# Optimization experiments

Measured on AMD Instinct MI355X. Metric: run time of the kernel, lower is better.

## Reference

```python
import jax, jax.numpy as jnp
import numpy as np

B, S, D, H = 2, 4096, 512, 8
HD = D // H  # 64


def setup_inputs() -> dict:
    key = jax.random.key(0)
    ks = jax.random.split(key, 9)
    def lin_init(kw, kb, fan_in, fan_out):
        bound = 1.0 / np.sqrt(fan_in)
        W = jax.random.uniform(kw, (fan_in, fan_out), minval=-bound, maxval=bound, dtype=jnp.float32)
        b = jax.random.uniform(kb, (fan_out,), minval=-bound, maxval=bound, dtype=jnp.float32)
        return W, b
    Wq, bq = lin_init(ks[0], ks[1], D, D)
    Wk, bk = lin_init(ks[2], ks[3], D, D)
    Wv, bv = lin_init(ks[4], ks[5], D, D)
    query = jax.random.normal(ks[6], (B, S, D), dtype=jnp.float32)
    key_in = jax.random.normal(ks[7], (B, S, D), dtype=jnp.float32)
    value = jax.random.normal(ks[8], (B, S, D), dtype=jnp.float32)
    return {"query": query, "key": key_in, "value": value,
            "Wq": Wq, "bq": bq, "Wk": Wk, "bk": bk, "Wv": Wv, "bv": bv}


def _split_heads(x):
    # [B, S, D] -> [B, H, S, HD]
    b, s, _ = x.shape
    return x.reshape(b, s, H, HD).transpose(0, 2, 1, 3)


def reference(query, key, value, Wq, bq, Wk, bk, Wv, bv):
    Q = _split_heads(query @ Wq + bq)
    K = _split_heads(key @ Wk + bk)
    V = _split_heads(value @ Wv + bv)
    scale = 1.0 / np.sqrt(HD).astype(np.float32)
    # scores: [B, H, Sq, Sk]
    scores = jnp.einsum('bhqd,bhkd->bhqk', Q, K) * scale
    weights = jax.nn.softmax(scores, axis=-1)
    att = jnp.einsum('bhqk,bhkd->bhqd', weights, V)
    # [B, H, S, HD] -> [B, S, D]
    return att.transpose(0, 2, 1, 3).reshape(query.shape[0], query.shape[1], D)
```

## Files before the change

kernel.cpp:

```cpp
#include <hip/hip_runtime.h>
#include <hip/hip_bf16.h>
#include <cstdint>


typedef __bf16   bf16x8 __attribute__((ext_vector_type(8)));
typedef _Float16 f16x8  __attribute__((ext_vector_type(8)));
typedef float    f32x4  __attribute__((ext_vector_type(4)));
typedef float    f32x16 __attribute__((ext_vector_type(16)));
typedef unsigned int   u32;
typedef unsigned int   u32x4 __attribute__((ext_vector_type(4)));
typedef unsigned short u16;

#define NB  2
#define SEQ 4096
#define DIM 512
#define NH  8
#define HD  64
#define WSZ (DIM * DIM)
#define QSZ (NB * NH * SEQ * HD)

__device__ __forceinline__ u16 f2bf(float f) {
    __bf16 h = (__bf16)f; return __builtin_bit_cast(u16, h);
}
__device__ __forceinline__ u16 f2h(float f) {
    _Float16 h = (_Float16)f; return __builtin_bit_cast(u16, h);
}
__device__ __forceinline__ bf16x8 cvt8(const float* s) {
    float4 a = *(const float4*)s, b = *(const float4*)(s + 4);
    bf16x8 o;
    o[0]=(__bf16)a.x; o[1]=(__bf16)a.y; o[2]=(__bf16)a.z; o[3]=(__bf16)a.w;
    o[4]=(__bf16)b.x; o[5]=(__bf16)b.y; o[6]=(__bf16)b.z; o[7]=(__bf16)b.w;
    return o;
}

__global__ __launch_bounds__(256) void wt_kernel(
    const float* __restrict__ Wq, const float* __restrict__ Wk,
    const float* __restrict__ Wv, u16* __restrict__ wt)
{
    __shared__ u16 lT[64 * 65];
    const int p = blockIdx.z;
    const float* W = (p == 0) ? Wq : ((p == 1) ? Wk : Wv);
    u16* dst = wt + (size_t)p * WSZ;
    const int r0 = blockIdx.x * 64, c0 = blockIdx.y * 64;
    const int t = threadIdx.x;
#pragma unroll
    for (int i = 0; i < 16; i++) {
        int idx = i * 256 + t, row = idx >> 6, col = idx & 63;
        lT[col * 65 + row] = f2bf(W[(size_t)(r0 + row) * DIM + c0 + col]);
    }
    __syncthreads();
#pragma unroll
    for (int i = 0; i < 16; i++) {
        int idx = i * 256 + t, n = idx >> 6, k = idx & 63;
        dst[(size_t)(c0 + n) * DIM + r0 + k] = lT[n * 65 + k];
    }
}

__global__ __launch_bounds__(256, 2) void proj_kernel(
    const float* __restrict__ xq, const float* __restrict__ xk,
    const float* __restrict__ xv, const u16* __restrict__ wt,
    const float* __restrict__ bq, const float* __restrict__ bk,
    const float* __restrict__ bv,
    u16* __restrict__ qb, u16* __restrict__ kb, u16* __restrict__ vt)
{
    __shared__ u16 lA[128 * 72];
    __shared__ u16 lB[256 * 72];

    const int tid = threadIdx.x;
    const int wave = tid >> 6, lane = tid & 63;
    const int l16 = lane & 15, quad = lane >> 4;
    const int wq = wave >> 1, wn = wave & 1;

    int p, mb, nb;
    {
        const int id = blockIdx.x;
        if (id < 256) { p = id >> 7; const int r = id & 127; mb = r >> 1; nb = r & 1; }
        else          { p = 2; const int r = id - 256; mb = r >> 5; nb = r & 31; }
    }
    const float* Xp = (p == 0) ? xq : ((p == 1) ? xk : xv);
    const u16*   Wp = wt + (size_t)p * WSZ;
    const bool cvtA = (p < 2);
    const float* Af = Xp + (size_t)mb * 128 * DIM;
    const u16*   Ab = Wp + (size_t)mb * 128 * DIM;
    const u16*   Bb = Wp + (size_t)nb * 256 * DIM;
    const float* Bf = Xp + (size_t)nb * 256 * DIM;

    f32x4 acc[4][8];
#pragma unroll
    for (int ms = 0; ms < 4; ms++)
#pragma unroll
        for (int ns = 0; ns < 8; ns++)
#pragma unroll
            for (int j = 0; j < 4; j++) acc[ms][ns][j] = 0.f;

    for (int kk = 0; kk < DIM; kk += 64) {
        __syncthreads();
#pragma unroll
        for (int i = 0; i < 4; i++) {
            const int c = i * 256 + tid, row = c >> 3, seg = c & 7;
            if (cvtA)
                *(bf16x8*)&lA[row * 72 + seg * 8] = cvt8(Af + (size_t)row * DIM + kk + seg * 8);
            else
                *(u32x4*)&lA[row * 72 + seg * 8] =
                    *(const u32x4*)(Ab + (size_t)row * DIM + kk + seg * 8);
        }
#pragma unroll
        for (int i = 0; i < 8; i++) {
            const int c = i * 256 + tid, row = c >> 3, seg = c & 7;
            if (cvtA)
                *(u32x4*)&lB[row * 72 + seg * 8] =
                    *(const u32x4*)(Bb + (size_t)row * DIM + kk + seg * 8);
            else
                *(bf16x8*)&lB[row * 72 + seg * 8] = cvt8(Bf + (size_t)row * DIM + kk + seg * 8);
        }
        __syncthreads();

        bf16x8 af[4][2];
#pragma unroll
        for (int ms = 0; ms < 4; ms++) {
            af[ms][0] = *(const bf16x8*)&lA[(wq * 64 + ms * 16 + l16) * 72 + quad * 8];
            af[ms][1] = *(const bf16x8*)&lA[(wq * 64 + ms * 16 + l16) * 72 + 32 + quad * 8];
        }
#pragma unroll
        for (int ns = 0; ns < 8; ns++) {
            bf16x8 b0 = *(const bf16x8*)&lB[(wn * 128 + ns * 16 + l16) * 72 + quad * 8];
            bf16x8 b1 = *(const bf16x8*)&lB[(wn * 128 + ns * 16 + l16) * 72 + 32 + quad * 8];
#pragma unroll
            for (int ms = 0; ms < 4; ms++) {
                acc[ms][ns] = __builtin_amdgcn_mfma_f32_16x16x32_bf16(af[ms][0], b0, acc[ms][ns], 0, 0, 0);
                acc[ms][ns] = __builtin_amdgcn_mfma_f32_16x16x32_bf16(af[ms][1], b1, acc[ms][ns], 0, 0, 0);
            }
        }
    }

    if (p < 2) {
        u16* dst = p ? kb : qb;
        const float* bias = p ? bk : bq;
        const float cs = (p == 0) ? 0.18033688011112042f : 1.0f;
#pragma unroll
        for (int ns = 0; ns < 8; ns++) {
            const int col = nb * 256 + wn * 128 + ns * 16 + l16;
            const int h = col >> 6, ch = col & 63;
            const float bval = bias[col];
#pragma unroll
            for (int ms = 0; ms < 4; ms++)
#pragma unroll
                for (int r = 0; r < 4; r++) {
                    const int m = mb * 128 + wq * 64 + ms * 16 + quad * 4 + r;
                    const int b = m >> 12, sq = m & (SEQ - 1);
                    dst[(((size_t)(b * NH + h) * SEQ + sq) << 6) + ch] =
                        f2bf((acc[ms][ns][r] + bval) * cs);
                }
        }
    } else {
#pragma unroll
        for (int ms = 0; ms < 4; ms++)
#pragma unroll
            for (int r = 0; r < 4; r++) {
                const int feat = mb * 128 + wq * 64 + ms * 16 + quad * 4 + r;
                const float bval = bv[feat];
                const int h = feat >> 6, hd = feat & 63;
#pragma unroll
                for (int ns = 0; ns < 8; ns++) {
                    const int n = nb * 256 + wn * 128 + ns * 16 + l16;
                    const int b = n >> 12, sq = n & (SEQ - 1);
                    vt[(((size_t)((b * NH + h) * HD + hd)) << 12) + sq] =
                        f2h(acc[ms][ns][r] + bval);
                }
            }
    }
}

__global__ __launch_bounds__(256) void attn_kernel(
    const u16* __restrict__ qb, const u16* __restrict__ kb,
    const u16* __restrict__ vt, float* __restrict__ out)
{
    __shared__ u16 sK[2][64 * 72];
    __shared__ u16 sV[2][64 * 72];

    const int tid = threadIdx.x;
    const int wave = tid >> 6, lane = tid & 63;
    const int m31 = lane & 31, h = lane >> 5;
    const int xsw = (m31 >> 3) & 3;

    const int blk = blockIdx.x;
    const int xcd = blk & 7, idx = blk >> 3;
    const int bh = xcd * 2 + (idx >> 4);
    const int qt = idx & 15;
    const int q0 = qt * 256 + wave * 64;

    const u16* Kb = kb + (size_t)bh * SEQ * HD;
    const u16* Vt = vt + (size_t)bh * HD * SEQ;

    bf16x8 qF[2][4];
#pragma unroll
    for (int qg = 0; qg < 2; qg++)
#pragma unroll
        for (int c = 0; c < 4; c++)
            qF[qg][c] = *(const bf16x8*)(qb + ((size_t)bh * SEQ + q0 + qg * 32 + m31) * HD
                                         + c * 16 + h * 8);

    f32x16 O[2][2];
#pragma unroll
    for (int qg = 0; qg < 2; qg++)
#pragma unroll
        for (int hg = 0; hg < 2; hg++)
#pragma unroll
            for (int j = 0; j < 16; j++) O[qg][hg][j] = 0.f;
    float l_acc[2] = {0.f, 0.f};

    u32x4 rK[1], rV[1];
    u32x4 rK1, rV1;

    {
        const int c0 = tid, c1 = 256 + tid;
        const int r0 = c0 >> 3, s0 = c0 & 7, g0 = s0 ^ ((r0 >> 3) & 3);
        const int r1 = c1 >> 3, s1 = c1 & 7, g1 = s1 ^ ((r1 >> 3) & 3);
        rK[0] = *(const u32x4*)(Kb + (((size_t)r0) << 6) + g0 * 8);
        rK1   = *(const u32x4*)(Kb + (((size_t)r1) << 6) + g1 * 8);
        rV[0] = *(const u32x4*)(Vt + (((size_t)r0) << 12) + g0 * 8);
        rV1   = *(const u32x4*)(Vt + (((size_t)r1) << 12) + g1 * 8);
        *(u32x4*)&sK[0][r0 * 72 + s0 * 8] = rK[0];
        *(u32x4*)&sK[0][r1 * 72 + s1 * 8] = rK1;
        *(u32x4*)&sV[0][r0 * 72 + s0 * 8] = rV[0];
        *(u32x4*)&sV[0][r1 * 72 + s1 * 8] = rV1;
    }

    for (int t = 0; t < SEQ / 64; t++) {
        __syncthreads();
        const int buf = t & 1;

        if (t < SEQ / 64 - 1) {
            const int k0n = (t + 1) << 6;
            const int c0 = tid, c1 = 256 + tid;
            const int r0 = c0 >> 3, s0 = c0 & 7, g0 = s0 ^ ((r0 >> 3) & 3);
            const int r1 = c1 >> 3, s1 = c1 & 7, g1 = s1 ^ ((r1 >> 3) & 3);
            rK[0] = *(const u32x4*)(Kb + (((size_t)(k0n + r0)) << 6) + g0 * 8);
            rK1   = *(const u32x4*)(Kb + (((size_t)(k0n + r1)) << 6) + g1 * 8);
            rV[0] = *(const u32x4*)(Vt + (((size_t)r0) << 12) + k0n + g0 * 8);
            rV1   = *(const u32x4*)(Vt + (((size_t)r1) << 12) + k0n + g1 * 8);
        }

#pragma unroll
        for (int kg = 0; kg < 2; kg++) {
            bf16x8 kA[4];
#pragma unroll
            for (int c = 0; c < 4; c++)
                kA[c] = *(const bf16x8*)&sK[buf][(kg * 32 + m31) * 72
                                                + (((2 * c + h) ^ xsw) << 3)];
            f16x8 vA[2][2];
#pragma unroll
            for (int hg = 0; hg < 2; hg++)
#pragma unroll
                for (int c2 = 0; c2 < 2; c2++)
                    vA[hg][c2] = *(const f16x8*)&sV[buf][(hg * 32 + m31) * 72
                                                + (((4 * kg + 2 * c2 + h) ^ xsw) << 3)];

#pragma unroll
            for (int qg = 0; qg < 2; qg++) {
                f32x16 St;
#pragma unroll
                for (int j = 0; j < 16; j++) St[j] = 0.f;
#pragma unroll
                for (int c = 0; c < 4; c++)
                    St = __builtin_amdgcn_mfma_f32_32x32x16_bf16(kA[c], qF[qg][c], St, 0, 0, 0);

                float ps = 0.f;
                u32 P32[8];
#pragma unroll
                for (int mm = 0; mm < 8; mm++) {
                    const float e0 = __builtin_amdgcn_exp2f(St[2 * mm]);
                    const float e1 = __builtin_amdgcn_exp2f(St[2 * mm + 1]);
                    ps += e0 + e1;
                    P32[mm] = (u32)f2h(e0) | ((u32)f2h(e1) << 16);
                }
                l_acc[qg] += ps;

                const bool hb = (h != 0);
                const u32 t0 = hb ? P32[0] : P32[2];  const u32 x0 = __shfl_xor(t0, 32);
                const u32 t1 = hb ? P32[1] : P32[3];  const u32 x1 = __shfl_xor(t1, 32);
                const u32 t2 = hb ? P32[4] : P32[6];  const u32 x2 = __shfl_xor(t2, 32);
                const u32 t3 = hb ? P32[5] : P32[7];  const u32 x3 = __shfl_xor(t3, 32);
                u32x4 f0, f1;
                f0[0] = hb ? x0 : P32[0];  f0[1] = hb ? x1 : P32[1];
                f0[2] = hb ? P32[2] : x0;  f0[3] = hb ? P32[3] : x1;
                f1[0] = hb ? x2 : P32[4];  f1[1] = hb ? x3 : P32[5];
                f1[2] = hb ? P32[6] : x2;  f1[3] = hb ? P32[7] : x3;
                const f16x8 pf0 = __builtin_bit_cast(f16x8, f0);
                const f16x8 pf1 = __builtin_bit_cast(f16x8, f1);
#pragma unroll
                for (int hg = 0; hg < 2; hg++) {
                    O[qg][hg] = __builtin_amdgcn_mfma_f32_32x32x16_f16(vA[hg][0], pf0, O[qg][hg], 0, 0, 0);
                    O[qg][hg] = __builtin_amdgcn_mfma_f32_32x32x16_f16(vA[hg][1], pf1, O[qg][hg], 0, 0, 0);
                }
            }
        }

        if (t < SEQ / 64 - 1) {
            const int c0 = tid, c1 = 256 + tid;
            const int r0 = c0 >> 3, s0 = c0 & 7;
            const int r1 = c1 >> 3, s1 = c1 & 7;
            *(u32x4*)&sK[buf ^ 1][r0 * 72 + s0 * 8] = rK[0];
            *(u32x4*)&sK[buf ^ 1][r1 * 72 + s1 * 8] = rK1;
            *(u32x4*)&sV[buf ^ 1][r0 * 72 + s0 * 8] = rV[0];
            *(u32x4*)&sV[buf ^ 1][r1 * 72 + s1 * 8] = rV1;
        }
    }

    const int b = bh >> 3, hcol = bh & 7;
#pragma unroll
    for (int qg = 0; qg < 2; qg++) {
        float lt = l_acc[qg];
        lt += __shfl_xor(lt, 32);
        const float inv = 1.0f / lt;
        const int sq = q0 + qg * 32 + m31;
#pragma unroll
        for (int hg = 0; hg < 2; hg++)
#pragma unroll
            for (int mm = 0; mm < 4; mm++) {
                f32x4 o;
#pragma unroll
                for (int j = 0; j < 4; j++) o[j] = O[qg][hg][4 * mm + j] * inv;
                *(f32x4*)&out[(((size_t)(b * SEQ + sq)) << 9) + hcol * 64
                              + hg * 32 + 8 * mm + 4 * h] = o;
            }
    }
}

extern "C" void kernel_launch(void* const* d_in, const int* in_sizes, int n_in,
                              void* d_out, int out_size, void* d_ws, size_t ws_size,
                              hipStream_t stream)
{
    const float* q  = (const float*)d_in[0];
    const float* k  = (const float*)d_in[1];
    const float* v  = (const float*)d_in[2];
    const float* Wq = (const float*)d_in[3];
    const float* bq = (const float*)d_in[4];
    const float* Wk = (const float*)d_in[5];
    const float* bk = (const float*)d_in[6];
    const float* Wv = (const float*)d_in[7];
    const float* bv = (const float*)d_in[8];
    float* out = (float*)d_out;

    u16* wt  = (u16*)d_ws;
    u16* qbp = wt  + (size_t)3 * WSZ;
    u16* kbp = qbp + (size_t)QSZ;
    u16* vtp = kbp + (size_t)QSZ;

    wt_kernel  <<<dim3(8, 8, 3), 256, 0, stream>>>(Wq, Wk, Wv, wt);
    proj_kernel<<<dim3(384),     256, 0, stream>>>(q, k, v, wt, bq, bk, bv,
                                                   qbp, kbp, vtp);
    attn_kernel<<<dim3(256),     256, 0, stream>>>(qbp, kbp, vtp, out);
}
```

Before: 250.8 us.

## Split attention KV range across waves and shrink projection tiles for more blocks

The attention kernel now splits the key sequence in half between wave pairs and doubles the block count to 512, merging the partial outputs and row sums through shared memory at the end. The V transpose layout is permuted at projection time so P packs directly into the MFMA operand, which removes the cross-half shuffles, and a packed pkrtz f16 conversion is used. The projection tile is halved in N (768 blocks) to raise parallelism. This trades extra shared memory, a final combine step and more K/V prefetch registers for better CU occupancy across the device.

```diff
diff --git a/kernel.cpp b/kernel.cpp
--- a/kernel.cpp
+++ b/kernel.cpp
@@ -24,6 +24,10 @@
 }
 __device__ __forceinline__ u16 f2h(float f) {
     _Float16 h = (_Float16)f; return __builtin_bit_cast(u16, h);
+}
+__device__ __forceinline__ u32 pack_pkrtz(float a, float b) {
+    auto pk = __builtin_amdgcn_cvt_pkrtz(a, b);
+    return __builtin_bit_cast(u32, pk);
 }
 __device__ __forceinline__ bf16x8 cvt8(const float* s) {
     float4 a = *(const float4*)s, b = *(const float4*)(s + 4);
@@ -56,7 +60,7 @@
     }
 }
 
-__global__ __launch_bounds__(256, 2) void proj_kernel(
+__global__ __launch_bounds__(256) void proj_kernel(
     const float* __restrict__ xq, const float* __restrict__ xk,
     const float* __restrict__ xv, const u16* __restrict__ wt,
     const float* __restrict__ bq, const float* __restrict__ bk,
@@ -64,7 +68,7 @@
     u16* __restrict__ qb, u16* __restrict__ kb, u16* __restrict__ vt)
 {
     __shared__ u16 lA[128 * 72];
-    __shared__ u16 lB[256 * 72];
+    __shared__ u16 lB[128 * 72];
 
     const int tid = threadIdx.x;
     const int wave = tid >> 6, lane = tid & 63;
@@ -74,22 +78,22 @@
     int p, mb, nb;
     {
         const int id = blockIdx.x;
-        if (id < 256) { p = id >> 7; const int r = id & 127; mb = r >> 1; nb = r & 1; }
-        else          { p = 2; const int r = id - 256; mb = r >> 5; nb = r & 31; }
+        if (id < 512) { p = id >> 8; const int r = id & 255; mb = r >> 2; nb = r & 3; }
+        else          { p = 2; const int r = id - 512; mb = r >> 6; nb = r & 63; }
     }
     const float* Xp = (p == 0) ? xq : ((p == 1) ? xk : xv);
     const u16*   Wp = wt + (size_t)p * WSZ;
     const bool cvtA = (p < 2);
     const float* Af = Xp + (size_t)mb * 128 * DIM;
     const u16*   Ab = Wp + (size_t)mb * 128 * DIM;
-    const u16*   Bb = Wp + (size_t)nb * 256 * DIM;
-    const float* Bf = Xp + (size_t)nb * 256 * DIM;
-
-    f32x4 acc[4][8];
+    const u16*   Bb = Wp + (size_t)nb * 128 * DIM;
+    const float* Bf = Xp + (size_t)nb * 128 * DIM;
+
+    f32x4 acc[4][4];
 #pragma unroll
     for (int ms = 0; ms < 4; ms++)
 #pragma unroll
-        for (int ns = 0; ns < 8; ns++)
+        for (int ns = 0; ns < 4; ns++)
 #pragma unroll
             for (int j = 0; j < 4; j++) acc[ms][ns][j] = 0.f;
 
@@ -105,7 +109,7 @@
                     *(const u32x4*)(Ab + (size_t)row * DIM + kk + seg * 8);
         }
 #pragma unroll
-        for (int i = 0; i < 8; i++) {
+        for (int i = 0; i < 4; i++) {
             const int c = i * 256 + tid, row = c >> 3, seg = c & 7;
             if (cvtA)
                 *(u32x4*)&lB[row * 72 + seg * 8] =
@@ -122,9 +126,9 @@
             af[ms][1] = *(const bf16x8*)&lA[(wq * 64 + ms * 16 + l16) * 72 + 32 + quad * 8];
         }
 #pragma unroll
-        for (int ns = 0; ns < 8; ns++) {
-            bf16x8 b0 = *(const bf16x8*)&lB[(wn * 128 + ns * 16 + l16) * 72 + quad * 8];
-            bf16x8 b1 = *(const bf16x8*)&lB[(wn * 128 + ns * 16 + l16) * 72 + 32 + quad * 8];
+        for (int ns = 0; ns < 4; ns++) {
+            bf16x8 b0 = *(const bf16x8*)&lB[(wn * 64 + ns * 16 + l16) * 72 + quad * 8];
+            bf16x8 b1 = *(const bf16x8*)&lB[(wn * 64 + ns * 16 + l16) * 72 + 32 + quad * 8];
 #pragma unroll
             for (int ms = 0; ms < 4; ms++) {
                 acc[ms][ns] = __builtin_amdgcn_mfma_f32_16x16x32_bf16(af[ms][0], b0, acc[ms][ns], 0, 0, 0);
@@ -137,11 +141,11 @@
         u16* dst = p ? kb : qb;
         const float* bias = p ? bk : bq;
         const float cs = (p == 0) ? 0.18033688011112042f : 1.0f;
-#pragma unroll
-        for (int ns = 0; ns < 8; ns++) {
-            const int col = nb * 256 + wn * 128 + ns * 16 + l16;
-            const int h = col >> 6, ch = col & 63;
-            const float bval = bias[col];
+        const int h = nb * 2 + wn;
+#pragma unroll
+        for (int ns = 0; ns < 4; ns++) {
+            const int ch = ns * 16 + l16;
+            const float bval = bias[h * 64 + ch];
 #pragma unroll
             for (int ms = 0; ms < 4; ms++)
 #pragma unroll
@@ -161,10 +165,11 @@
                 const float bval = bv[feat];
                 const int h = feat >> 6, hd = feat & 63;
 #pragma unroll
-                for (int ns = 0; ns < 8; ns++) {
-                    const int n = nb * 256 + wn * 128 + ns * 16 + l16;
+                for (int ns = 0; ns < 4; ns++) {
+                    const int n = nb * 128 + wn * 64 + ns * 16 + l16;
                     const int b = n >> 12, sq = n & (SEQ - 1);
-                    vt[(((size_t)((b * NH + h) * HD + hd)) << 12) + sq] =
+                    const int sqp = (sq & ~12) | ((sq & 8) >> 1) | ((sq & 4) << 1);
+                    vt[(((size_t)((b * NH + h) * HD + hd)) << 12) + sqp] =
                         f2h(acc[ms][ns][r] + bval);
                 }
             }
@@ -175,19 +180,20 @@
     const u16* __restrict__ qb, const u16* __restrict__ kb,
     const u16* __restrict__ vt, float* __restrict__ out)
 {
-    __shared__ u16 sK[2][64 * 72];
-    __shared__ u16 sV[2][64 * 72];
+    __shared__ u16 smem[2 * 2 * 2 * 64 * 72];
+    float* cmb = (float*)smem;
 
     const int tid = threadIdx.x;
     const int wave = tid >> 6, lane = tid & 63;
     const int m31 = lane & 31, h = lane >> 5;
     const int xsw = (m31 >> 3) & 3;
+    const int wq = wave >> 1, kh = wave & 1;
 
     const int blk = blockIdx.x;
     const int xcd = blk & 7, idx = blk >> 3;
-    const int bh = xcd * 2 + (idx >> 4);
-    const int qt = idx & 15;
-    const int q0 = qt * 256 + wave * 64;
+    const int bh = xcd * 2 + (idx >> 5);
+    const int qt = idx & 31;
+    const int qbase = qt * 128 + wq * 64;
 
     const u16* Kb = kb + (size_t)bh * SEQ * HD;
     const u16* Vt = vt + (size_t)bh * HD * SEQ;
@@ -197,7 +203,7 @@
     for (int qg = 0; qg < 2; qg++)
 #pragma unroll
         for (int c = 0; c < 4; c++)
-            qF[qg][c] = *(const bf16x8*)(qb + ((size_t)bh * SEQ + q0 + qg * 32 + m31) * HD
+            qF[qg][c] = *(const bf16x8*)(qb + ((size_t)bh * SEQ + qbase + qg * 32 + m31) * HD
                                          + c * 16 + h * 8);
 
     f32x16 O[2][2];
@@ -209,36 +215,38 @@
             for (int j = 0; j < 16; j++) O[qg][hg][j] = 0.f;
     float l_acc[2] = {0.f, 0.f};
 
-    u32x4 rK[1], rV[1];
-    u32x4 rK1, rV1;
-
-    {
-        const int c0 = tid, c1 = 256 + tid;
-        const int r0 = c0 >> 3, s0 = c0 & 7, g0 = s0 ^ ((r0 >> 3) & 3);
-        const int r1 = c1 >> 3, s1 = c1 & 7, g1 = s1 ^ ((r1 >> 3) & 3);
-        rK[0] = *(const u32x4*)(Kb + (((size_t)r0) << 6) + g0 * 8);
-        rK1   = *(const u32x4*)(Kb + (((size_t)r1) << 6) + g1 * 8);
-        rV[0] = *(const u32x4*)(Vt + (((size_t)r0) << 12) + g0 * 8);
-        rV1   = *(const u32x4*)(Vt + (((size_t)r1) << 12) + g1 * 8);
-        *(u32x4*)&sK[0][r0 * 72 + s0 * 8] = rK[0];
-        *(u32x4*)&sK[0][r1 * 72 + s1 * 8] = rK1;
-        *(u32x4*)&sV[0][r0 * 72 + s0 * 8] = rV[0];
-        *(u32x4*)&sV[0][r1 * 72 + s1 * 8] = rV1;
-    }
-
-    for (int t = 0; t < SEQ / 64; t++) {
+    u32x4 pf[8];
+#pragma unroll
+    for (int e = 0; e < 8; e++) {
+        const int g = e * 256 + tid;
+        const int tt = g >> 9, w = g & 511;
+        const int kh_t = tt >> 1, kv = tt & 1;
+        const int row = w >> 3, seg = w & 7, gs = seg ^ ((row >> 3) & 3);
+        const int kb0 = kh_t * (SEQ / 2);
+        pf[e] = kv ? *(const u32x4*)(Vt + (((size_t)row) << 12) + kb0 + gs * 8)
+                   : *(const u32x4*)(Kb + (((size_t)(kb0 + row)) << 6) + gs * 8);
+        *(u32x4*)&smem[(size_t)tt * (64 * 72) + row * 72 + seg * 8] = pf[e];
+    }
+
+    const int NT = (SEQ / 2) / 64;
+    for (int it = 0; it < NT; it++) {
         __syncthreads();
-        const int buf = t & 1;
-
-        if (t < SEQ / 64 - 1) {
-            const int k0n = (t + 1) << 6;
-            const int c0 = tid, c1 = 256 + tid;
-            const int r0 = c0 >> 3, s0 = c0 & 7, g0 = s0 ^ ((r0 >> 3) & 3);
-            const int r1 = c1 >> 3, s1 = c1 & 7, g1 = s1 ^ ((r1 >> 3) & 3);
-            rK[0] = *(const u32x4*)(Kb + (((size_t)(k0n + r0)) << 6) + g0 * 8);
-            rK1   = *(const u32x4*)(Kb + (((size_t)(k0n + r1)) << 6) + g1 * 8);
-            rV[0] = *(const u32x4*)(Vt + (((size_t)r0) << 12) + k0n + g0 * 8);
-            rV1   = *(const u32x4*)(Vt + (((size_t)r1) << 12) + k0n + g1 * 8);
+        const int buf = it & 1;
+        const u16* sK = &smem[((size_t)(buf * 2 + kh) * 2 + 0) * (64 * 72)];
+        const u16* sV = &smem[((size_t)(buf * 2 + kh) * 2 + 1) * (64 * 72)];
+
+        if (it + 1 < NT) {
+#pragma unroll
+            for (int e = 0; e < 8; e++) {
+                const int g = e * 256 + tid;
+                const int tt = g >> 9, kv = tt & 1;
+                const int kh_t = tt >> 1;
+                const int w = g & 511;
+                const int row = w >> 3, seg = w & 7, gs = seg ^ ((row >> 3) & 3);
+                const int k0 = kh_t * (SEQ / 2) + (it + 1) * 64;
+                pf[e] = kv ? *(const u32x4*)(Vt + (((size_t)row) << 12) + k0 + gs * 8)
+                           : *(const u32x4*)(Kb + (((size_t)(k0 + row)) << 6) + gs * 8);
+            }
         }
 
 #pragma unroll
@@ -246,15 +254,14 @@
             bf16x8 kA[4];
 #pragma unroll
             for (int c = 0; c < 4; c++)
-                kA[c] = *(const bf16x8*)&sK[buf][(kg * 32 + m31) * 72
-                                                + (((2 * c + h) ^ xsw) << 3)];
+                kA[c] = *(const bf16x8*)&sK[(kg * 32 + m31) * 72 + (((2 * c + h) ^ xsw) << 3)];
             f16x8 vA[2][2];
 #pragma unroll
             for (int hg = 0; hg < 2; hg++)
 #pragma unroll
                 for (int c2 = 0; c2 < 2; c2++)
-                    vA[hg][c2] = *(const f16x8*)&sV[buf][(hg * 32 + m31) * 72
-                                                + (((4 * kg + 2 * c2 + h) ^ xsw) << 3)];
+                    vA[hg][c2] = *(const f16x8*)&sV[(hg * 32 + m31) * 72
+                                                    + (((4 * kg + 2 * c2 + h) ^ xsw) << 3)];
 
 #pragma unroll
             for (int qg = 0; qg < 2; qg++) {
@@ -272,20 +279,13 @@
                     const float e0 = __builtin_amdgcn_exp2f(St[2 * mm]);
                     const float e1 = __builtin_amdgcn_exp2f(St[2 * mm + 1]);
                     ps += e0 + e1;
-                    P32[mm] = (u32)f2h(e0) | ((u32)f2h(e1) << 16);
+                    P32[mm] = pack_pkrtz(e0, e1);
                 }
                 l_acc[qg] += ps;
 
-                const bool hb = (h != 0);
-                const u32 t0 = hb ? P32[0] : P32[2];  const u32 x0 = __shfl_xor(t0, 32);
-                const u32 t1 = hb ? P32[1] : P32[3];  const u32 x1 = __shfl_xor(t1, 32);
-                const u32 t2 = hb ? P32[4] : P32[6];  const u32 x2 = __shfl_xor(t2, 32);
-                const u32 t3 = hb ? P32[5] : P32[7];  const u32 x3 = __shfl_xor(t3, 32);
                 u32x4 f0, f1;
-                f0[0] = hb ? x0 : P32[0];  f0[1] = hb ? x1 : P32[1];
-                f0[2] = hb ? P32[2] : x0;  f0[3] = hb ? P32[3] : x1;
-                f1[0] = hb ? x2 : P32[4];  f1[1] = hb ? x3 : P32[5];
-                f1[2] = hb ? P32[6] : x2;  f1[3] = hb ? P32[7] : x3;
+                f0[0] = P32[0]; f0[1] = P32[1]; f0[2] = P32[2]; f0[3] = P32[3];
+                f1[0] = P32[4]; f1[1] = P32[5]; f1[2] = P32[6]; f1[3] = P32[7];
                 const f16x8 pf0 = __builtin_bit_cast(f16x8, f0);
                 const f16x8 pf1 = __builtin_bit_cast(f16x8, f1);
 #pragma unroll
@@ -296,34 +296,58 @@
             }
         }
 
-        if (t < SEQ / 64 - 1) {
-            const int c0 = tid, c1 = 256 + tid;
-            const int r0 = c0 >> 3, s0 = c0 & 7;
-            const int r1 = c1 >> 3, s1 = c1 & 7;
-            *(u32x4*)&sK[buf ^ 1][r0 * 72 + s0 * 8] = rK[0];
-            *(u32x4*)&sK[buf ^ 1][r1 * 72 + s1 * 8] = rK1;
-            *(u32x4*)&sV[buf ^ 1][r0 * 72 + s0 * 8] = rV[0];
-            *(u32x4*)&sV[buf ^ 1][r1 * 72 + s1 * 8] = rV1;
-        }
-    }
-
-    const int b = bh >> 3, hcol = bh & 7;
-#pragma unroll
-    for (int qg = 0; qg < 2; qg++) {
-        float lt = l_acc[qg];
-        lt += __shfl_xor(lt, 32);
-        const float inv = 1.0f / lt;
-        const int sq = q0 + qg * 32 + m31;
-#pragma unroll
-        for (int hg = 0; hg < 2; hg++)
-#pragma unroll
-            for (int mm = 0; mm < 4; mm++) {
-                f32x4 o;
-#pragma unroll
-                for (int j = 0; j < 4; j++) o[j] = O[qg][hg][4 * mm + j] * inv;
-                *(f32x4*)&out[(((size_t)(b * SEQ + sq)) << 9) + hcol * 64
-                              + hg * 32 + 8 * mm + 4 * h] = o;
-            }
+        if (it + 1 < NT) {
+            u16* dstb = &smem[(size_t)((buf ^ 1) * 4) * (64 * 72)];
+#pragma unroll
+            for (int e = 0; e < 8; e++) {
+                const int g = e * 256 + tid;
+                const int tt = g >> 9, w = g & 511;
+                const int row = w >> 3, seg = w & 7;
+                *(u32x4*)&dstb[(size_t)tt * (64 * 72) + row * 72 + seg * 8] = pf[e];
+            }
+        }
+    }
+
+#pragma unroll
+    for (int qg = 0; qg < 2; qg++) l_acc[qg] += __shfl_xor(l_acc[qg], 32);
+
+    __syncthreads();
+    if (kh == 1) {
+#pragma unroll
+        for (int qg = 0; qg < 2; qg++) {
+#pragma unroll
+            for (int hg = 0; hg < 2; hg++)
+#pragma unroll
+                for (int mm = 0; mm < 4; mm++) {
+                    f32x4 o;
+#pragma unroll
+                    for (int j = 0; j < 4; j++) o[j] = O[qg][hg][4 * mm + j];
+                    *(f32x4*)&cmb[((((wq * 2 + qg) * 2 + hg) * 4 + mm) << 8) + lane * 4] = o;
+                }
+            cmb[32 * 256 + (wq * 2 + qg) * 64 + lane] = l_acc[qg];
+        }
+    }
+    __syncthreads();
+
+    if (kh == 0) {
+        const int b = bh >> 3, hcol = bh & 7;
+#pragma unroll
+        for (int qg = 0; qg < 2; qg++) {
+            const float lt = l_acc[qg] + cmb[32 * 256 + (wq * 2 + qg) * 64 + lane];
+            const float inv = 1.0f / lt;
+            const int sq = qbase + qg * 32 + m31;
+#pragma unroll
+            for (int hg = 0; hg < 2; hg++)
+#pragma unroll
+                for (int mm = 0; mm < 4; mm++) {
+                    const f32x4 po = *(const f32x4*)&cmb[((((wq * 2 + qg) * 2 + hg) * 4 + mm) << 8) + lane * 4];
+                    f32x4 o;
+#pragma unroll
+                    for (int j = 0; j < 4; j++) o[j] = (O[qg][hg][4 * mm + j] + po[j]) * inv;
+                    *(f32x4*)&out[(((size_t)(b * SEQ + sq)) << 9) + hcol * 64
+                                  + hg * 32 + 8 * mm + 4 * h] = o;
+                }
+        }
     }
 }
 
@@ -348,7 +372,7 @@
     u16* vtp = kbp + (size_t)QSZ;
 
     wt_kernel  <<<dim3(8, 8, 3), 256, 0, stream>>>(Wq, Wk, Wv, wt);
-    proj_kernel<<<dim3(384),     256, 0, stream>>>(q, k, v, wt, bq, bk, bv,
+    proj_kernel<<<dim3(768),     256, 0, stream>>>(q, k, v, wt, bq, bk, bv,
                                                    qbp, kbp, vtp);
-    attn_kernel<<<dim3(256),     256, 0, stream>>>(qbp, kbp, vtp, out);
-}
+    attn_kernel<<<dim3(512),     256, 0, stream>>>(qbp, kbp, vtp, out);
+}
```

Result: no change. 254.6 us (+1.5%).
